# Performance work log

Hardware: AMD Instinct MI355X
Metric: run time of the kernel (lower is better)

The kernel has to match this reference:

```python
import jax, jax.numpy as jnp
import numpy as np

CR = 32  # channels // reduction

def setup_inputs() -> dict:
    key = jax.random.key(0)
    k1, k2 = jax.random.split(key)
    x = jax.random.normal(k1, (1, 64, 8, 32, 32), dtype=jnp.float32)
    W = jax.random.normal(k2, (CR, 64), dtype=jnp.float32) * (1.0 / np.sqrt(64.0))
    bias = jnp.zeros((CR,), dtype=jnp.float32)
    return {"x": x, "W": W, "bias": bias}

def reference(x, W, bias):
    b, c, d, h, w = x.shape
    cr = W.shape[0]
    n = d * h * w
    # 1x1x1 Conv3d == per-voxel linear projection over channels
    x_red = jnp.einsum('oc,bcdhw->bodhw', W, x) + bias[None, :, None, None, None]
    q = x_red.reshape(b, cr, n)          # [b, cr, N]
    k = q                                 # shared projection (q == k)
    v = x.reshape(b, c, n)               # [b, c, N]
    # attn[b, i, j] = <q[:, i], k[:, j]>, softmax over j (dim=2)
    attn = jnp.einsum('bci,bcj->bij', q, k) / jnp.sqrt(jnp.float32(cr))
    attn = jax.nn.softmax(attn, axis=2)
    # out[b, c, m] = sum_n v[b, c, n] * attn[b, n, m]  (torch.bmm(v, attn))
    out = jnp.einsum('bcn,bnm->bcm', v, attn)
    out = out.reshape(b, c, d, h, w)
    return out + x
```

## Files before the change

### kernel.cpp

```cpp
#include <hip/hip_runtime.h>

#define N_TOK 8192

typedef _Float16 f16x8 __attribute__((ext_vector_type(8)));
typedef _Float16 f16x4 __attribute__((ext_vector_type(4)));
typedef float    f32x4 __attribute__((ext_vector_type(4)));

__device__ __forceinline__ f32x4 mfma_k32(f16x8 a, f16x8 b, f32x4 c) {
  return __builtin_amdgcn_mfma_f32_16x16x32_f16(a, b, c, 0, 0, 0);
}
__device__ __forceinline__ f32x4 mfma_k16(f16x4 a, f16x4 b, f32x4 c) {
  return __builtin_amdgcn_mfma_f32_16x16x16f16(a, b, c, 0, 0, 0);
}

#define QSCALE 0.50500977f

__global__ __launch_bounds__(256) void prep_kernel(
    const float* __restrict__ x, const float* __restrict__ W,
    const float* __restrict__ bias, _Float16* __restrict__ qe,
    _Float16* __restrict__ vht) {
  int blk = blockIdx.x, t = threadIdx.x;
  if (blk < 1024) {
    __shared__ float Wl[32 * 65];
    for (int i = t; i < 2048; i += 256) Wl[(i >> 6) * 65 + (i & 63)] = W[i];
    __syncthreads();
    int g = blk * 256 + t;
    int o = g & 31, n = g >> 5;
    float acc0 = bias[o], acc1 = 0.f;
#pragma unroll
    for (int c = 0; c < 32; ++c) {
      acc0 = fmaf(Wl[o * 65 + c], x[c * N_TOK + n], acc0);
      acc1 = fmaf(Wl[o * 65 + 32 + c], x[(32 + c) * N_TOK + n], acc1);
    }
    qe[n * 32 + o] = (_Float16)((acc0 + acc1) * QSCALE);
  } else {
    int i = (blk - 1024) * 256 + t;
    f32x4 v = ((const f32x4*)x)[i];
    f16x4 hv;
#pragma unroll
    for (int j = 0; j < 4; ++j) hv[j] = (_Float16)v[j];
    int c = i >> 11, n4 = i & 2047;
    int nblk = n4 >> 3, k = n4 & 7, q = k & 3, h = k >> 2;
    *(f16x4*)(vht + nblk * 2048 + c * 32 + q * 8 + h * 4) = hv;
  }
}

__global__ __launch_bounds__(1024) void pass1_kernel(
    const _Float16* __restrict__ qe, float* __restrict__ Bn) {
  __shared__ float Lp[16][32];
  int t = threadIdx.x;
  int w = t >> 6, lane = t & 63, quad = lane >> 4, l15 = lane & 15;
  int n0 = blockIdx.x * 32;
  f16x8 af0 = *(const f16x8*)(qe + (n0 + l15) * 32 + quad * 8);
  f16x8 af1 = *(const f16x8*)(qe + (n0 + 16 + l15) * 32 + quad * 8);
  f32x4 sums0 = {0.f, 0.f, 0.f, 0.f}, sums1 = {0.f, 0.f, 0.f, 0.f};
  for (int mt = 0; mt < 16; ++mt) {
    int m0 = w * 512 + mt * 32;
    f16x8 bf0 = *(const f16x8*)(qe + (m0 + l15) * 32 + quad * 8);
    f16x8 bf1 = *(const f16x8*)(qe + (m0 + 16 + l15) * 32 + quad * 8);
    f32x4 zero = {0.f, 0.f, 0.f, 0.f};
    f32x4 s00 = mfma_k32(af0, bf0, zero);
    f32x4 s01 = mfma_k32(af0, bf1, zero);
    f32x4 s10 = mfma_k32(af1, bf0, zero);
    f32x4 s11 = mfma_k32(af1, bf1, zero);
#pragma unroll
    for (int r = 0; r < 4; ++r) {
      sums0[r] += __builtin_amdgcn_exp2f(s00[r]) + __builtin_amdgcn_exp2f(s01[r]);
      sums1[r] += __builtin_amdgcn_exp2f(s10[r]) + __builtin_amdgcn_exp2f(s11[r]);
    }
  }
#pragma unroll
  for (int r = 0; r < 4; ++r) {
#pragma unroll
    for (int mask = 1; mask < 16; mask <<= 1) {
      sums0[r] += __shfl_xor(sums0[r], mask, 64);
      sums1[r] += __shfl_xor(sums1[r], mask, 64);
    }
  }
  if (l15 == 0) {
    *(f32x4*)&Lp[w][quad * 4] = sums0;
    *(f32x4*)&Lp[w][16 + quad * 4] = sums1;
  }
  __syncthreads();
  if (t < 32) {
    float L = 0.f;
#pragma unroll
    for (int ww = 0; ww < 16; ++ww) L += Lp[ww][t];
    Bn[n0 + t] = __builtin_amdgcn_logf(L);
  }
}

__global__ __launch_bounds__(1024) void pass2_kernel(
    const _Float16* __restrict__ qe, const _Float16* __restrict__ vht,
    const float* __restrict__ Bn, const float* __restrict__ x,
    float* __restrict__ out) {
  __shared__ float Ot[8 * 64 * 33];
  int t = threadIdx.x;
  int w = t >> 6, lane = t & 63, quad = lane >> 4, l15 = lane & 15;
  int m0 = blockIdx.x * 32;

  f16x8 bm0 = *(const f16x8*)(qe + (m0 + l15) * 32 + quad * 8);
  f16x8 bm1 = *(const f16x8*)(qe + (m0 + 16 + l15) * 32 + quad * 8);

  f32x4 acc[4][2];
#pragma unroll
  for (int ct = 0; ct < 4; ++ct)
#pragma unroll
    for (int mt = 0; mt < 2; ++mt) acc[ct][mt] = f32x4{0.f, 0.f, 0.f, 0.f};

  f16x8 anA0, anA1, avA[4];
  f32x4 BqA0, BqA1;
  f16x8 anB0, anB1, avB[4];
  f32x4 BqB0, BqB1;

#define LOADCH(SUF, NB)                                                     \
  do {                                                                      \
    int nb_ = (NB);                                                         \
    an##SUF##0 = *(const f16x8*)(qe + (nb_ + l15) * 32 + quad * 8);         \
    an##SUF##1 = *(const f16x8*)(qe + (nb_ + 16 + l15) * 32 + quad * 8);    \
    Bq##SUF##0 = *(const f32x4*)(Bn + nb_ + quad * 4);                      \
    Bq##SUF##1 = *(const f32x4*)(Bn + nb_ + 16 + quad * 4);                 \
    const _Float16* vb_ = vht + (nb_ >> 5) * 2048 + l15 * 32 + quad * 8;    \
    _Pragma("unroll") for (int ct = 0; ct < 4; ++ct) av##SUF[ct] =          \
        *(const f16x8*)(vb_ + ct * 512);                                    \
  } while (0)

#define COMPUTECH(SUF)                                                      \
  do {                                                                      \
    f32x4 zero = {0.f, 0.f, 0.f, 0.f};                                      \
    f32x4 s00 = mfma_k32(an##SUF##0, bm0, zero);     \
    f32x4 s01 = mfma_k32(an##SUF##0, bm1, zero);              \
    f32x4 s10 = mfma_k32(an##SUF##1, bm0, zero);         \
    f32x4 s11 = mfma_k32(an##SUF##1, bm1, zero);                            \
    f16x4 p00, p01, p10, p11;                                               \
    _Pragma("unroll") for (int r = 0; r < 4; ++r) {                         \
      p00[r] = (_Float16)__builtin_amdgcn_exp2f(s00[r] - Bq##SUF##0[r]);    \
      p01[r] = (_Float16)__builtin_amdgcn_exp2f(s01[r] - Bq##SUF##0[r]);    \
      p10[r] = (_Float16)__builtin_amdgcn_exp2f(s10[r] - Bq##SUF##1[r]);    \
      p11[r] = (_Float16)__builtin_amdgcn_exp2f(s11[r] - Bq##SUF##1[r]);    \
    }                                                                       \
    _Pragma("unroll") for (int ct = 0; ct < 4; ++ct) {                      \
      f16x4 lo, hi;                                                         \
      _Pragma("unroll") for (int j = 0; j < 4; ++j) {                       \
        lo[j] = av##SUF[ct][j];                                             \
        hi[j] = av##SUF[ct][j + 4];                                         \
      }                                                                     \
      acc[ct][0] = mfma_k16(lo, p00, acc[ct][0]);                           \
      acc[ct][0] = mfma_k16(hi, p10, acc[ct][0]);                           \
      acc[ct][1] = mfma_k16(lo, p01, acc[ct][1]);                           \
      acc[ct][1] = mfma_k16(hi, p11, acc[ct][1]);                           \
    }                                                                       \
  } while (0)

  int nbase = w * 512;
  LOADCH(A, nbase);
  for (int ch2 = 0; ch2 < 8; ++ch2) {
    int nb = nbase + ch2 * 64;
    LOADCH(B, nb + 32);
    COMPUTECH(A);
    if (ch2 < 7) LOADCH(A, nb + 64);
    COMPUTECH(B);
  }
#undef LOADCH
#undef COMPUTECH

  if (w < 8) {
#pragma unroll
    for (int ct = 0; ct < 4; ++ct)
#pragma unroll
      for (int mt = 0; mt < 2; ++mt)
#pragma unroll
        for (int r = 0; r < 4; ++r)
          Ot[(w * 64 + ct * 16 + quad * 4 + r) * 33 + mt * 16 + l15] =
              acc[ct][mt][r];
  }
  __syncthreads();
  if (w >= 8) {
#pragma unroll
    for (int ct = 0; ct < 4; ++ct)
#pragma unroll
      for (int mt = 0; mt < 2; ++mt)
#pragma unroll
        for (int r = 0; r < 4; ++r)
          Ot[((w - 8) * 64 + ct * 16 + quad * 4 + r) * 33 + mt * 16 + l15] +=
              acc[ct][mt][r];
  }
  __syncthreads();
  for (int idx = t; idx < 2048; idx += 1024) {
    int cc = idx >> 5, m = idx & 31;
    float v = 0.f;
#pragma unroll
    for (int s = 0; s < 8; ++s) v += Ot[(s * 64 + cc) * 33 + m];
    out[cc * N_TOK + m0 + m] = v + x[cc * N_TOK + m0 + m];
  }
}

extern "C" void kernel_launch(void* const* d_in, const int* in_sizes, int n_in,
                              void* d_out, int out_size, void* d_ws,
                              size_t ws_size, hipStream_t stream) {
  const float* x = (const float*)d_in[0];
  const float* W = (const float*)d_in[1];
  const float* bias = (const float*)d_in[2];
  float* out = (float*)d_out;

  char* ws = (char*)d_ws;
  _Float16* qe = (_Float16*)ws;
  _Float16* vht = (_Float16*)(ws + 524288);
  float* Bn = (float*)(ws + 524288 + 1048576);

  prep_kernel<<<1536, 256, 0, stream>>>(x, W, bias, qe, vht);
  pass1_kernel<<<256, 1024, 0, stream>>>(qe, Bn);
  pass2_kernel<<<256, 1024, 0, stream>>>(qe, vht, Bn, x, out);
}
```

Before: 102.0 us.

## Fuse prep, pass1 and pass2 into one cooperative kernel with grid syncs

Merges the three launches into a single cooperative kernel of 256 blocks that uses grid.sync between the projection, the softmax-denominator pass and the output pass. The projection now stages x in shared memory per block and produces vht in the same step. Shared memory is reused through a union. The goal is to remove launch gaps and inter-kernel drain, at the cost of grid-wide barriers and a prep stage that now runs with only 256 blocks of 1024 threads.

Result: slower. 279.6 us (+174.2%).

```diff
diff --git a/kernel.cpp b/kernel.cpp
--- a/kernel.cpp
+++ b/kernel.cpp
@@ -1,4 +1,7 @@
 #include <hip/hip_runtime.h>
+#include <hip/hip_cooperative_groups.h>
+
+namespace cg = cooperative_groups;
 
 #define N_TOK 8192
 
@@ -15,183 +18,193 @@
 
 #define QSCALE 0.50500977f
 
-__global__ __launch_bounds__(256) void prep_kernel(
+__global__ __launch_bounds__(1024) void fused_kernel(
     const float* __restrict__ x, const float* __restrict__ W,
     const float* __restrict__ bias, _Float16* __restrict__ qe,
-    _Float16* __restrict__ vht) {
-  int blk = blockIdx.x, t = threadIdx.x;
-  if (blk < 1024) {
-    __shared__ float Wl[32 * 65];
-    for (int i = t; i < 2048; i += 256) Wl[(i >> 6) * 65 + (i & 63)] = W[i];
-    __syncthreads();
-    int g = blk * 256 + t;
-    int o = g & 31, n = g >> 5;
-    float acc0 = bias[o], acc1 = 0.f;
+    _Float16* __restrict__ vht, float* __restrict__ Bn,
+    float* __restrict__ out) {
+  __shared__ union {
+    struct {
+      float Wl[32 * 65];
+      float xl[64 * 36];
+    } p1;
+    float Lp[16][32];
+    float Ot[8 * 64 * 33];
+  } sm;
+
+  cg::grid_group grid = cg::this_grid();
+  int t = threadIdx.x;
+  int b = blockIdx.x;
+  int n0 = b * 32;
+  int w = t >> 6, lane = t & 63, quad = lane >> 4, l15 = lane & 15;
+
+  for (int i = t; i < 2048; i += 1024)
+    sm.p1.Wl[(i >> 6) * 65 + (i & 63)] = W[i];
+  if (t < 512) {
+    int c = t >> 3, j4 = t & 7;
+    f32x4 v = *(const f32x4*)(x + c * N_TOK + n0 + j4 * 4);
+    *(f32x4*)&sm.p1.xl[c * 36 + j4 * 4] = v;
+    f16x4 hv;
+#pragma unroll
+    for (int j = 0; j < 4; ++j) hv[j] = (_Float16)v[j];
+    int q = j4 & 3, h = j4 >> 2;
+    *(f16x4*)(vht + b * 2048 + c * 32 + q * 8 + h * 4) = hv;
+  }
+  __syncthreads();
+  {
+    int nl = t >> 5, o = t & 31;
+    float a0 = bias[o], a1 = 0.f;
 #pragma unroll
     for (int c = 0; c < 32; ++c) {
-      acc0 = fmaf(Wl[o * 65 + c], x[c * N_TOK + n], acc0);
-      acc1 = fmaf(Wl[o * 65 + 32 + c], x[(32 + c) * N_TOK + n], acc1);
-    }
-    qe[n * 32 + o] = (_Float16)((acc0 + acc1) * QSCALE);
-  } else {
-    int i = (blk - 1024) * 256 + t;
-    f32x4 v = ((const f32x4*)x)[i];
-    f16x4 hv;
-#pragma unroll
-    for (int j = 0; j < 4; ++j) hv[j] = (_Float16)v[j];
-    int c = i >> 11, n4 = i & 2047;
-    int nblk = n4 >> 3, k = n4 & 7, q = k & 3, h = k >> 2;
-    *(f16x4*)(vht + nblk * 2048 + c * 32 + q * 8 + h * 4) = hv;
-  }
-}
-
-__global__ __launch_bounds__(1024) void pass1_kernel(
-    const _Float16* __restrict__ qe, float* __restrict__ Bn) {
-  __shared__ float Lp[16][32];
-  int t = threadIdx.x;
-  int w = t >> 6, lane = t & 63, quad = lane >> 4, l15 = lane & 15;
-  int n0 = blockIdx.x * 32;
-  f16x8 af0 = *(const f16x8*)(qe + (n0 + l15) * 32 + quad * 8);
-  f16x8 af1 = *(const f16x8*)(qe + (n0 + 16 + l15) * 32 + quad * 8);
-  f32x4 sums0 = {0.f, 0.f, 0.f, 0.f}, sums1 = {0.f, 0.f, 0.f, 0.f};
-  for (int mt = 0; mt < 16; ++mt) {
-    int m0 = w * 512 + mt * 32;
-    f16x8 bf0 = *(const f16x8*)(qe + (m0 + l15) * 32 + quad * 8);
-    f16x8 bf1 = *(const f16x8*)(qe + (m0 + 16 + l15) * 32 + quad * 8);
-    f32x4 zero = {0.f, 0.f, 0.f, 0.f};
-    f32x4 s00 = mfma_k32(af0, bf0, zero);
-    f32x4 s01 = mfma_k32(af0, bf1, zero);
-    f32x4 s10 = mfma_k32(af1, bf0, zero);
-    f32x4 s11 = mfma_k32(af1, bf1, zero);
+      a0 = fmaf(sm.p1.Wl[o * 65 + c], sm.p1.xl[c * 36 + nl], a0);
+      a1 = fmaf(sm.p1.Wl[o * 65 + 32 + c], sm.p1.xl[(32 + c) * 36 + nl], a1);
+    }
+    qe[(n0 + nl) * 32 + o] = (_Float16)((a0 + a1) * QSCALE);
+  }
+  __threadfence();
+  grid.sync();
+
+  {
+    f16x8 af0 = *(const f16x8*)(qe + (n0 + l15) * 32 + quad * 8);
+    f16x8 af1 = *(const f16x8*)(qe + (n0 + 16 + l15) * 32 + quad * 8);
+    f32x4 sums0 = {0.f, 0.f, 0.f, 0.f}, sums1 = {0.f, 0.f, 0.f, 0.f};
+    for (int mt = 0; mt < 16; ++mt) {
+      int m0 = w * 512 + mt * 32;
+      f16x8 bf0 = *(const f16x8*)(qe + (m0 + l15) * 32 + quad * 8);
+      f16x8 bf1 = *(const f16x8*)(qe + (m0 + 16 + l15) * 32 + quad * 8);
+      f32x4 zero = {0.f, 0.f, 0.f, 0.f};
+      f32x4 s00 = mfma_k32(af0, bf0, zero);
+      f32x4 s01 = mfma_k32(af0, bf1, zero);
+      f32x4 s10 = mfma_k32(af1, bf0, zero);
+      f32x4 s11 = mfma_k32(af1, bf1, zero);
+#pragma unroll
+      for (int r = 0; r < 4; ++r) {
+        sums0[r] +=
+            __builtin_amdgcn_exp2f(s00[r]) + __builtin_amdgcn_exp2f(s01[r]);
+        sums1[r] +=
+            __builtin_amdgcn_exp2f(s10[r]) + __builtin_amdgcn_exp2f(s11[r]);
+      }
+    }
 #pragma unroll
     for (int r = 0; r < 4; ++r) {
-      sums0[r] += __builtin_amdgcn_exp2f(s00[r]) + __builtin_amdgcn_exp2f(s01[r]);
-      sums1[r] += __builtin_amdgcn_exp2f(s10[r]) + __builtin_amdgcn_exp2f(s11[r]);
-    }
-  }
-#pragma unroll
-  for (int r = 0; r < 4; ++r) {
-#pragma unroll
-    for (int mask = 1; mask < 16; mask <<= 1) {
-      sums0[r] += __shfl_xor(sums0[r], mask, 64);
-      sums1[r] += __shfl_xor(sums1[r], mask, 64);
-    }
-  }
-  if (l15 == 0) {
-    *(f32x4*)&Lp[w][quad * 4] = sums0;
-    *(f32x4*)&Lp[w][16 + quad * 4] = sums1;
-  }
-  __syncthreads();
-  if (t < 32) {
-    float L = 0.f;
-#pragma unroll
-    for (int ww = 0; ww < 16; ++ww) L += Lp[ww][t];
-    Bn[n0 + t] = __builtin_amdgcn_logf(L);
-  }
-}
-
-__global__ __launch_bounds__(1024) void pass2_kernel(
-    const _Float16* __restrict__ qe, const _Float16* __restrict__ vht,
-    const float* __restrict__ Bn, const float* __restrict__ x,
-    float* __restrict__ out) {
-  __shared__ float Ot[8 * 64 * 33];
-  int t = threadIdx.x;
-  int w = t >> 6, lane = t & 63, quad = lane >> 4, l15 = lane & 15;
-  int m0 = blockIdx.x * 32;
-
-  f16x8 bm0 = *(const f16x8*)(qe + (m0 + l15) * 32 + quad * 8);
-  f16x8 bm1 = *(const f16x8*)(qe + (m0 + 16 + l15) * 32 + quad * 8);
-
-  f32x4 acc[4][2];
-#pragma unroll
-  for (int ct = 0; ct < 4; ++ct)
-#pragma unroll
-    for (int mt = 0; mt < 2; ++mt) acc[ct][mt] = f32x4{0.f, 0.f, 0.f, 0.f};
-
-  f16x8 anA0, anA1, avA[4];
-  f32x4 BqA0, BqA1;
-  f16x8 anB0, anB1, avB[4];
-  f32x4 BqB0, BqB1;
-
-#define LOADCH(SUF, NB)                                                     \
-  do {                                                                      \
-    int nb_ = (NB);                                                         \
-    an##SUF##0 = *(const f16x8*)(qe + (nb_ + l15) * 32 + quad * 8);         \
-    an##SUF##1 = *(const f16x8*)(qe + (nb_ + 16 + l15) * 32 + quad * 8);    \
-    Bq##SUF##0 = *(const f32x4*)(Bn + nb_ + quad * 4);                      \
-    Bq##SUF##1 = *(const f32x4*)(Bn + nb_ + 16 + quad * 4);                 \
-    const _Float16* vb_ = vht + (nb_ >> 5) * 2048 + l15 * 32 + quad * 8;    \
-    _Pragma("unroll") for (int ct = 0; ct < 4; ++ct) av##SUF[ct] =          \
-        *(const f16x8*)(vb_ + ct * 512);                                    \
+#pragma unroll
+      for (int mask = 1; mask < 16; mask <<= 1) {
+        sums0[r] += __shfl_xor(sums0[r], mask, 64);
+        sums1[r] += __shfl_xor(sums1[r], mask, 64);
+      }
+    }
+    if (l15 == 0) {
+      *(f32x4*)&sm.Lp[w][quad * 4] = sums0;
+      *(f32x4*)&sm.Lp[w][16 + quad * 4] = sums1;
+    }
+    __syncthreads();
+    if (t < 32) {
+      float L = 0.f;
+#pragma unroll
+      for (int ww = 0; ww < 16; ++ww) L += sm.Lp[ww][t];
+      Bn[n0 + t] = __builtin_amdgcn_logf(L);
+    }
+  }
+  __threadfence();
+  grid.sync();
+
+  {
+    int m0 = n0;
+    f16x8 bm0 = *(const f16x8*)(qe + (m0 + l15) * 32 + quad * 8);
+    f16x8 bm1 = *(const f16x8*)(qe + (m0 + 16 + l15) * 32 + quad * 8);
+
+    f32x4 acc[4][2];
+#pragma unroll
+    for (int ct = 0; ct < 4; ++ct)
+#pragma unroll
+      for (int mt = 0; mt < 2; ++mt) acc[ct][mt] = f32x4{0.f, 0.f, 0.f, 0.f};
+
+    f16x8 anA0, anA1, avA[4];
+    f32x4 BqA0, BqA1;
+    f16x8 anB0, anB1, avB[4];
+    f32x4 BqB0, BqB1;
+
+#define LOADCH(SUF, NB)                                                    \
+  do {                                                                     \
+    int nb_ = (NB);                                                        \
+    an##SUF##0 = *(const f16x8*)(qe + (nb_ + l15) * 32 + quad * 8);        \
+    an##SUF##1 = *(const f16x8*)(qe + (nb_ + 16 + l15) * 32 + quad * 8);   \
+    Bq##SUF##0 = *(const f32x4*)(Bn + nb_ + quad * 4);                     \
+    Bq##SUF##1 = *(const f32x4*)(Bn + nb_ + 16 + quad * 4);                \
+    const _Float16* vb_ = vht + (nb_ >> 5) * 2048 + l15 * 32 + quad * 8;   \
+    _Pragma("unroll") for (int ct = 0; ct < 4; ++ct) av##SUF[ct] =         \
+        *(const f16x8*)(vb_ + ct * 512);                                   \
   } while (0)
 
-#define COMPUTECH(SUF)                                                      \
-  do {                                                                      \
-    f32x4 zero = {0.f, 0.f, 0.f, 0.f};                                      \
-    f32x4 s00 = mfma_k32(an##SUF##0, bm0, zero);     \
-    f32x4 s01 = mfma_k32(an##SUF##0, bm1, zero);              \
-    f32x4 s10 = mfma_k32(an##SUF##1, bm0, zero);         \
-    f32x4 s11 = mfma_k32(an##SUF##1, bm1, zero);                            \
-    f16x4 p00, p01, p10, p11;                                               \
-    _Pragma("unroll") for (int r = 0; r < 4; ++r) {                         \
-      p00[r] = (_Float16)__builtin_amdgcn_exp2f(s00[r] - Bq##SUF##0[r]);    \
-      p01[r] = (_Float16)__builtin_amdgcn_exp2f(s01[r] - Bq##SUF##0[r]);    \
-      p10[r] = (_Float16)__builtin_amdgcn_exp2f(s10[r] - Bq##SUF##1[r]);    \
-      p11[r] = (_Float16)__builtin_amdgcn_exp2f(s11[r] - Bq##SUF##1[r]);    \
-    }                                                                       \
-    _Pragma("unroll") for (int ct = 0; ct < 4; ++ct) {                      \
-      f16x4 lo, hi;                                                         \
-      _Pragma("unroll") for (int j = 0; j < 4; ++j) {                       \
-        lo[j] = av##SUF[ct][j];                                             \
-        hi[j] = av##SUF[ct][j + 4];                                         \
-      }                                                                     \
-      acc[ct][0] = mfma_k16(lo, p00, acc[ct][0]);                           \
-      acc[ct][0] = mfma_k16(hi, p10, acc[ct][0]);                           \
-      acc[ct][1] = mfma_k16(lo, p01, acc[ct][1]);                           \
-      acc[ct][1] = mfma_k16(hi, p11, acc[ct][1]);                           \
-    }                                                                       \
+#define COMPUTECH(SUF)                                                     \
+  do {                                                                     \
+    f32x4 zero = {0.f, 0.f, 0.f, 0.f};                                     \
+    f32x4 s00 = mfma_k32(an##SUF##0, bm0, zero);                           \
+    f32x4 s01 = mfma_k32(an##SUF##0, bm1, zero);                           \
+    f32x4 s10 = mfma_k32(an##SUF##1, bm0, zero);                           \
+    f32x4 s11 = mfma_k32(an##SUF##1, bm1, zero);                           \
+    f16x4 p00, p01, p10, p11;                                              \
+    _Pragma("unroll") for (int r = 0; r < 4; ++r) {                        \
+      p00[r] = (_Float16)__builtin_amdgcn_exp2f(s00[r] - Bq##SUF##0[r]);   \
+      p01[r] = (_Float16)__builtin_amdgcn_exp2f(s01[r] - Bq##SUF##0[r]);   \
+      p10[r] = (_Float16)__builtin_amdgcn_exp2f(s10[r] - Bq##SUF##1[r]);   \
+      p11[r] = (_Float16)__builtin_amdgcn_exp2f(s11[r] - Bq##SUF##1[r]);   \
+    }                                                                      \
+    _Pragma("unroll") for (int ct = 0; ct < 4; ++ct) {                     \
+      f16x4 lo, hi;                                                        \
+      _Pragma("unroll") for (int j = 0; j < 4; ++j) {                      \
+        lo[j] = av##SUF[ct][j];                                            \
+        hi[j] = av##SUF[ct][j + 4];                                        \
+      }                                                                    \
+      acc[ct][0] = mfma_k16(lo, p00, acc[ct][0]);                          \
+      acc[ct][0] = mfma_k16(hi, p10, acc[ct][0]);                          \
+      acc[ct][1] = mfma_k16(lo, p01, acc[ct][1]);                          \
+      acc[ct][1] = mfma_k16(hi, p11, acc[ct][1]);                          \
+    }                                                                      \
   } while (0)
 
-  int nbase = w * 512;
-  LOADCH(A, nbase);
-  for (int ch2 = 0; ch2 < 8; ++ch2) {
-    int nb = nbase + ch2 * 64;
-    LOADCH(B, nb + 32);
-    COMPUTECH(A);
-    if (ch2 < 7) LOADCH(A, nb + 64);
-    COMPUTECH(B);
-  }
+    int nbase = w * 512;
+    LOADCH(A, nbase);
+    for (int ch2 = 0; ch2 < 8; ++ch2) {
+      int nb = nbase + ch2 * 64;
+      LOADCH(B, nb + 32);
+      COMPUTECH(A);
+      if (ch2 < 7) LOADCH(A, nb + 64);
+      COMPUTECH(B);
+    }
 #undef LOADCH
 #undef COMPUTECH
 
-  if (w < 8) {
-#pragma unroll
-    for (int ct = 0; ct < 4; ++ct)
-#pragma unroll
-      for (int mt = 0; mt < 2; ++mt)
-#pragma unroll
-        for (int r = 0; r < 4; ++r)
-          Ot[(w * 64 + ct * 16 + quad * 4 + r) * 33 + mt * 16 + l15] =
-              acc[ct][mt][r];
-  }
-  __syncthreads();
-  if (w >= 8) {
-#pragma unroll
-    for (int ct = 0; ct < 4; ++ct)
-#pragma unroll
-      for (int mt = 0; mt < 2; ++mt)
-#pragma unroll
-        for (int r = 0; r < 4; ++r)
-          Ot[((w - 8) * 64 + ct * 16 + quad * 4 + r) * 33 + mt * 16 + l15] +=
-              acc[ct][mt][r];
-  }
-  __syncthreads();
-  for (int idx = t; idx < 2048; idx += 1024) {
-    int cc = idx >> 5, m = idx & 31;
-    float v = 0.f;
-#pragma unroll
-    for (int s = 0; s < 8; ++s) v += Ot[(s * 64 + cc) * 33 + m];
-    out[cc * N_TOK + m0 + m] = v + x[cc * N_TOK + m0 + m];
+    __syncthreads();
+    if (w < 8) {
+#pragma unroll
+      for (int ct = 0; ct < 4; ++ct)
+#pragma unroll
+        for (int mt = 0; mt < 2; ++mt)
+#pragma unroll
+          for (int r = 0; r < 4; ++r)
+            sm.Ot[(w * 64 + ct * 16 + quad * 4 + r) * 33 + mt * 16 + l15] =
+                acc[ct][mt][r];
+    }
+    __syncthreads();
+    if (w >= 8) {
+#pragma unroll
+      for (int ct = 0; ct < 4; ++ct)
+#pragma unroll
+        for (int mt = 0; mt < 2; ++mt)
+#pragma unroll
+          for (int r = 0; r < 4; ++r)
+            sm.Ot[((w - 8) * 64 + ct * 16 + quad * 4 + r) * 33 + mt * 16 +
+                  l15] += acc[ct][mt][r];
+    }
+    __syncthreads();
+    for (int idx = t; idx < 2048; idx += 1024) {
+      int cc = idx >> 5, m = idx & 31;
+      float v = 0.f;
+#pragma unroll
+      for (int s = 0; s < 8; ++s) v += sm.Ot[(s * 64 + cc) * 33 + m];
+      out[cc * N_TOK + m0 + m] = v + x[cc * N_TOK + m0 + m];
+    }
   }
 }
 
@@ -208,7 +221,8 @@
   _Float16* vht = (_Float16*)(ws + 524288);
   float* Bn = (float*)(ws + 524288 + 1048576);
 
-  prep_kernel<<<1536, 256, 0, stream>>>(x, W, bias, qe, vht);
-  pass1_kernel<<<256, 1024, 0, stream>>>(qe, Bn);
-  pass2_kernel<<<256, 1024, 0, stream>>>(qe, vht, Bn, x, out);
-}
+  void* args[] = {(void*)&x,   (void*)&W,  (void*)&bias, (void*)&qe,
+                  (void*)&vht, (void*)&Bn, (void*)&out};
+  hipLaunchCooperativeKernel((const void*)fused_kernel, dim3(256), dim3(1024),
+                             args, 0, stream);
+}
```

## Stage x tiles in LDS for projection, software-pipeline pass1 loads, add occupancy hints

Applied to the files above, without the earlier changes.

The prep kernel now gives each block a 32-token tile. The block loads x for all 64 channels into shared memory once, writes the fp16 V layout from that tile, and computes the Q projection from LDS instead of making 32 strided global reads per thread. Pass1 gets double-buffered loads of the key fragments so the global loads overlap the MFMA and exp work. Both attention kernels also get a minimum-blocks launch-bounds hint, which may force register caps and risks spills.

New measurement: 119.4 us. 1.17x slower.

```diff
diff --git a/kernel.cpp b/kernel.cpp
--- a/kernel.cpp
+++ b/kernel.cpp
@@ -15,37 +15,38 @@
 
 #define QSCALE 0.50500977f
 
-__global__ __launch_bounds__(256) void prep_kernel(
+__global__ __launch_bounds__(1024) void prep_kernel(
     const float* __restrict__ x, const float* __restrict__ W,
     const float* __restrict__ bias, _Float16* __restrict__ qe,
     _Float16* __restrict__ vht) {
-  int blk = blockIdx.x, t = threadIdx.x;
-  if (blk < 1024) {
-    __shared__ float Wl[32 * 65];
-    for (int i = t; i < 2048; i += 256) Wl[(i >> 6) * 65 + (i & 63)] = W[i];
-    __syncthreads();
-    int g = blk * 256 + t;
-    int o = g & 31, n = g >> 5;
-    float acc0 = bias[o], acc1 = 0.f;
-#pragma unroll
-    for (int c = 0; c < 32; ++c) {
-      acc0 = fmaf(Wl[o * 65 + c], x[c * N_TOK + n], acc0);
-      acc1 = fmaf(Wl[o * 65 + 32 + c], x[(32 + c) * N_TOK + n], acc1);
-    }
-    qe[n * 32 + o] = (_Float16)((acc0 + acc1) * QSCALE);
-  } else {
-    int i = (blk - 1024) * 256 + t;
-    f32x4 v = ((const f32x4*)x)[i];
+  __shared__ float Wl[32 * 65];
+  __shared__ float xl[64 * 36];
+  int t = threadIdx.x, b = blockIdx.x;
+  int n0 = b * 32;
+  for (int i = t; i < 2048; i += 1024)
+    Wl[(i >> 6) * 65 + (i & 63)] = W[i];
+  if (t < 512) {
+    int c = t >> 3, j4 = t & 7;
+    f32x4 v = *(const f32x4*)(x + c * N_TOK + n0 + j4 * 4);
+    *(f32x4*)&xl[c * 36 + j4 * 4] = v;
     f16x4 hv;
 #pragma unroll
     for (int j = 0; j < 4; ++j) hv[j] = (_Float16)v[j];
-    int c = i >> 11, n4 = i & 2047;
-    int nblk = n4 >> 3, k = n4 & 7, q = k & 3, h = k >> 2;
-    *(f16x4*)(vht + nblk * 2048 + c * 32 + q * 8 + h * 4) = hv;
-  }
-}
-
-__global__ __launch_bounds__(1024) void pass1_kernel(
+    int q = j4 & 3, h = j4 >> 2;
+    *(f16x4*)(vht + b * 2048 + c * 32 + q * 8 + h * 4) = hv;
+  }
+  __syncthreads();
+  int nl = t >> 5, o = t & 31;
+  float a0 = bias[o], a1 = 0.f;
+#pragma unroll
+  for (int c = 0; c < 32; ++c) {
+    a0 = fmaf(Wl[o * 65 + c], xl[c * 36 + nl], a0);
+    a1 = fmaf(Wl[o * 65 + 32 + c], xl[(32 + c) * 36 + nl], a1);
+  }
+  qe[(n0 + nl) * 32 + o] = (_Float16)((a0 + a1) * QSCALE);
+}
+
+__global__ __launch_bounds__(1024, 4) void pass1_kernel(
     const _Float16* __restrict__ qe, float* __restrict__ Bn) {
   __shared__ float Lp[16][32];
   int t = threadIdx.x;
@@ -54,21 +55,39 @@
   f16x8 af0 = *(const f16x8*)(qe + (n0 + l15) * 32 + quad * 8);
   f16x8 af1 = *(const f16x8*)(qe + (n0 + 16 + l15) * 32 + quad * 8);
   f32x4 sums0 = {0.f, 0.f, 0.f, 0.f}, sums1 = {0.f, 0.f, 0.f, 0.f};
-  for (int mt = 0; mt < 16; ++mt) {
-    int m0 = w * 512 + mt * 32;
-    f16x8 bf0 = *(const f16x8*)(qe + (m0 + l15) * 32 + quad * 8);
-    f16x8 bf1 = *(const f16x8*)(qe + (m0 + 16 + l15) * 32 + quad * 8);
-    f32x4 zero = {0.f, 0.f, 0.f, 0.f};
-    f32x4 s00 = mfma_k32(af0, bf0, zero);
-    f32x4 s01 = mfma_k32(af0, bf1, zero);
-    f32x4 s10 = mfma_k32(af1, bf0, zero);
-    f32x4 s11 = mfma_k32(af1, bf1, zero);
-#pragma unroll
-    for (int r = 0; r < 4; ++r) {
-      sums0[r] += __builtin_amdgcn_exp2f(s00[r]) + __builtin_amdgcn_exp2f(s01[r]);
-      sums1[r] += __builtin_amdgcn_exp2f(s10[r]) + __builtin_amdgcn_exp2f(s11[r]);
+  int mbase = w * 512;
+  f16x8 bfA0, bfA1, bfB0, bfB1;
+  bfA0 = *(const f16x8*)(qe + (mbase + l15) * 32 + quad * 8);
+  bfA1 = *(const f16x8*)(qe + (mbase + 16 + l15) * 32 + quad * 8);
+
+#define P1_STEP(BF0, BF1)                                                   \
+  do {                                                                      \
+    f32x4 zero = {0.f, 0.f, 0.f, 0.f};                                      \
+    f32x4 s00 = mfma_k32(af0, BF0, zero);                                   \
+    f32x4 s01 = mfma_k32(af0, BF1, zero);                                   \
+    f32x4 s10 = mfma_k32(af1, BF0, zero);                                   \
+    f32x4 s11 = mfma_k32(af1, BF1, zero);                                   \
+    _Pragma("unroll") for (int r = 0; r < 4; ++r) {                         \
+      sums0[r] +=                                                           \
+          __builtin_amdgcn_exp2f(s00[r]) + __builtin_amdgcn_exp2f(s01[r]);  \
+      sums1[r] +=                                                           \
+          __builtin_amdgcn_exp2f(s10[r]) + __builtin_amdgcn_exp2f(s11[r]);  \
+    }                                                                       \
+  } while (0)
+
+  for (int mt2 = 0; mt2 < 8; ++mt2) {
+    int m0 = mbase + mt2 * 64;
+    bfB0 = *(const f16x8*)(qe + (m0 + 32 + l15) * 32 + quad * 8);
+    bfB1 = *(const f16x8*)(qe + (m0 + 48 + l15) * 32 + quad * 8);
+    P1_STEP(bfA0, bfA1);
+    if (mt2 < 7) {
+      bfA0 = *(const f16x8*)(qe + (m0 + 64 + l15) * 32 + quad * 8);
+      bfA1 = *(const f16x8*)(qe + (m0 + 80 + l15) * 32 + quad * 8);
     }
-  }
+    P1_STEP(bfB0, bfB1);
+  }
+#undef P1_STEP
+
 #pragma unroll
   for (int r = 0; r < 4; ++r) {
 #pragma unroll
@@ -90,7 +109,7 @@
   }
 }
 
-__global__ __launch_bounds__(1024) void pass2_kernel(
+__global__ __launch_bounds__(1024, 4) void pass2_kernel(
     const _Float16* __restrict__ qe, const _Float16* __restrict__ vht,
     const float* __restrict__ Bn, const float* __restrict__ x,
     float* __restrict__ out) {
@@ -208,7 +227,7 @@
   _Float16* vht = (_Float16*)(ws + 524288);
   float* Bn = (float*)(ws + 524288 + 1048576);
 
-  prep_kernel<<<1536, 256, 0, stream>>>(x, W, bias, qe, vht);
+  prep_kernel<<<256, 1024, 0, stream>>>(x, W, bias, qe, vht);
   pass1_kernel<<<256, 1024, 0, stream>>>(qe, Bn);
   pass2_kernel<<<256, 1024, 0, stream>>>(qe, vht, Bn, x, out);
 }
```
